# Performance work log

Measured on AMD Instinct MI355X. Metric: run time of the kernel, lower is better.

Reference implementation:

```python
import jax, jax.numpy as jnp
import numpy as np


def setup_inputs() -> dict:
    key = jax.random.key(0)
    k1, k2 = jax.random.split(key)
    B, N, C, Hq, Wq = 4, 10, 256, 32, 32
    Hs, Ws = 32, 32
    return {
        "query_features": jax.random.normal(k1, (B, C, Hq, Wq), dtype=jnp.float32),
        "support_features": jax.random.normal(k2, (N, C, Hs, Ws), dtype=jnp.float32),
        "K": 5,
    }


def reference(query_features, support_features, K):
    B, C, Hq, Wq = query_features.shape
    N, _, Hs, Ws = support_features.shape
    Lq, Ls = Hq * Wq, Hs * Ws

    # [B, Lq, C] -> repeat over N -> [B*N, Lq, C]
    q = query_features.reshape(B, C, Lq).transpose(0, 2, 1)
    q = jnp.broadcast_to(q[:, None], (B, N, Lq, C)).reshape(B * N, Lq, C)
    # [N, C, Ls] -> repeat over B -> [B*N, C, Ls]
    s = support_features.reshape(N, C, Ls)
    s = jnp.broadcast_to(s[None], (B, N, C, Ls)).reshape(B * N, C, Ls)

    # global mean-centering (scalar mean over the whole repeated tensor)
    q = q - q.mean()
    s = s - s.mean()

    # unscaled similarity attention: QK^T -> softmax -> PV
    sim = jnp.einsum("bqc,bcs->bqs", q, s)          # [B*N, Lq, Ls]
    sim = jax.nn.softmax(sim, axis=-1)
    aligned = jnp.einsum("bqs,bcs->bqc", sim, s)    # [B*N, Lq, C]

    # average over K shots per class
    aligned = aligned.reshape(B, N // K, K, Hq, Wq, C).mean(axis=2)
    aligned = aligned.transpose(1, 0, 4, 2, 3)      # [N//K, B, C, Hq, Wq]

    q_out = q.transpose(0, 2, 1).reshape(B, N // K, K, C, Hq, Wq).mean(axis=2)
    # q_out: [B, N//K, C, Hq, Wq]
    return q_out, aligned
```

## Files before the change

### kernel.cpp

```cpp
#include <hip/hip_runtime.h>

#define CQ_ELEMS (4 * 256 * 1024)
#define CS_ELEMS (10 * 256 * 1024)
#define OUT2_OFF 2097152

typedef __attribute__((ext_vector_type(8))) _Float16 f16x8;
typedef __attribute__((ext_vector_type(4))) float f32x4;

#define WS_SH 256
#define SH_ELEMS (10 * 1024 * 256)
#define SV_ELEMS (10 * 256 * 1024)

__device__ __forceinline__ void gload_lds16(const unsigned short* g, unsigned short* l) {
    __builtin_amdgcn_global_load_lds(
        (const __attribute__((address_space(1))) void*)g,
        (__attribute__((address_space(3))) void*)l, 16, 0, 0);
}

__global__ __launch_bounds__(256) void means_kernel(const float* __restrict__ q,
                                                    const float* __restrict__ s,
                                                    float* __restrict__ ws) {
    const int tid = blockIdx.x * 256 + threadIdx.x;
    const int stride = gridDim.x * 256;
    float sq = 0.f, ss = 0.f;
    const float4* q4 = (const float4*)q;
    const float4* s4 = (const float4*)s;
    for (int i = tid; i < CQ_ELEMS / 4; i += stride) {
        float4 v = q4[i];
        sq += (v.x + v.y) + (v.z + v.w);
    }
    for (int i = tid; i < CS_ELEMS / 4; i += stride) {
        float4 v = s4[i];
        ss += (v.x + v.y) + (v.z + v.w);
    }
#pragma unroll
    for (int off = 32; off > 0; off >>= 1) {
        sq += __shfl_down(sq, off, 64);
        ss += __shfl_down(ss, off, 64);
    }
    __shared__ float redq[4], reds[4];
    const int lane = threadIdx.x & 63, wid = threadIdx.x >> 6;
    if (lane == 0) { redq[wid] = sq; reds[wid] = ss; }
    __syncthreads();
    if (threadIdx.x == 0) {
        atomicAdd(&ws[0], (redq[0] + redq[1]) + (redq[2] + redq[3]));
        atomicAdd(&ws[1], (reds[0] + reds[1]) + (reds[2] + reds[3]));
    }
}

__global__ __launch_bounds__(256) void convert_kernel(const float* __restrict__ Q,
                                                      const float* __restrict__ S,
                                                      const float* __restrict__ ws,
                                                      unsigned short* __restrict__ sh,
                                                      unsigned short* __restrict__ sv,
                                                      unsigned short* __restrict__ qt,
                                                      float* __restrict__ out) {
    __shared__ unsigned short Th[32][40];
    const int t = threadIdx.x;
    const int x0 = blockIdx.x << 5;
    const int c0 = blockIdx.y << 5;
    const int z = blockIdx.z;

    const int cl = t >> 3, x4 = (t & 7) << 2;

    if (z < 10) {
        const int n = z;
        const float ms = ws[1] * (1.0f / (float)CS_ELEMS);
        float4 v = *(const float4*)(S + ((size_t)(n * 256 + c0 + cl)) * 1024 + x0 + x4);
        float x[4] = {v.x - ms, v.y - ms, v.z - ms, v.w - ms};
        unsigned short hb[4];
#pragma unroll
        for (int j = 0; j < 4; ++j) {
            _Float16 h = (_Float16)x[j];
            hb[j] = __builtin_bit_cast(unsigned short, h);
            Th[cl][x4 + j] = hb[j];
        }
        *(ushort4*)(sv + ((size_t)(n * 256 + c0 + cl)) * 1024 + x0 + x4) =
            make_ushort4(hb[0], hb[1], hb[2], hb[3]);
        {
            const int lin = (z * 8 + blockIdx.y) * 32 + blockIdx.x;
            const int gid = lin * 256 + t;
            if (gid < 524288) ((int4*)(out + OUT2_OFF))[gid] = make_int4(0, 0, 0, 0);
        }
        __syncthreads();
        const int sl = t >> 3, c4 = (t & 7) << 2;
        *(ushort4*)(sh + ((size_t)(n * 1024 + x0 + sl)) * 256 + c0 + c4) =
            make_ushort4(Th[c4 + 0][sl], Th[c4 + 1][sl], Th[c4 + 2][sl], Th[c4 + 3][sl]);
    } else {
        const int b = z - 10;
        const float mq = ws[0] * (1.0f / (float)CQ_ELEMS);
        float4 v = *(const float4*)(Q + ((size_t)(b * 256 + c0 + cl)) * 1024 + x0 + x4);
        v.x -= mq; v.y -= mq; v.z -= mq; v.w -= mq;
        float* o = out + ((size_t)(b * 2) * 256 + (c0 + cl)) * 1024 + x0 + x4;
        *(float4*)o = v;
        *(float4*)(o + 256 * 1024) = v;
        float x[4] = {v.x, v.y, v.z, v.w};
#pragma unroll
        for (int j = 0; j < 4; ++j) {
            _Float16 h = (_Float16)x[j];
            Th[cl][x4 + j] = __builtin_bit_cast(unsigned short, h);
        }
        __syncthreads();
        const int ql = t >> 3, c4 = (t & 7) << 2;
        *(ushort4*)(qt + ((size_t)(b * 1024 + x0 + ql)) * 256 + c0 + c4) =
            make_ushort4(Th[c4 + 0][ql], Th[c4 + 1][ql], Th[c4 + 2][ql], Th[c4 + 3][ql]);
    }
}

union __align__(16) SMem {
    struct {
        unsigned short s1[8192];
        unsigned short s2[8192];
        unsigned short pb[64][40];
    } st;
    float epi[2][64][68];
};

__global__ __launch_bounds__(256, 3) void attn_kernel(const unsigned short* __restrict__ qt,
                                                      const unsigned short* __restrict__ sh,
                                                      const unsigned short* __restrict__ sv,
                                                      float* __restrict__ out) {
    __shared__ SMem sm;

    const int t = threadIdx.x;
    const int w = t >> 6;
    const int lane = t & 63;
    const int quad = lane >> 4;
    const int l16 = lane & 15;

    const int q0 = blockIdx.x << 6;
    const int bn = blockIdx.y;
    const int b = bn / 10;
    const int n = bn - b * 10;
    const int g = n / 5;

    const unsigned short* __restrict__ Shn = sh + (size_t)n * (1024 * 256);
    const unsigned short* __restrict__ Svn = sv + (size_t)n * (256 * 1024);

    f16x8 qf[8];
    {
        const unsigned short* qp = qt + (size_t)(b * 1024 + q0 + 16 * w + l16) * 256 + quad * 8;
#pragma unroll
        for (int f = 0; f < 8; ++f)
            qf[f] = *(const f16x8*)(qp + f * 32);
    }

    f32x4 O[4][4];
#pragma unroll
    for (int mt = 0; mt < 4; ++mt)
#pragma unroll
        for (int nt = 0; nt < 4; ++nt) O[mt][nt] = (f32x4){0.f, 0.f, 0.f, 0.f};

    float m_run[4], l_run[4];
#pragma unroll
    for (int r = 0; r < 4; ++r) { m_run[r] = -1e30f; l_run[r] = 0.f; }

    for (int s0i = 0; s0i < 32; ++s0i) {
        const int s0 = s0i << 5;
        __syncthreads();

#pragma unroll
        for (int j = 0; j < 4; ++j) {
            const int fidx = 4 * w + j;
            const unsigned short* g1 = Shn +
                (size_t)(s0 + 2 * (lane & 15) + (fidx & 1)) * 256 + (fidx >> 1) * 32 + (lane >> 4) * 8;
            gload_lds16(g1, &sm.st.s1[fidx * 512]);
            const unsigned short* g2 = Svn +
                (size_t)(w * 64 + j * 16 + (lane >> 2)) * 1024 + s0 + ((lane & 3) ^ (lane >> 4)) * 8;
            gload_lds16(g2, &sm.st.s2[fidx * 512]);
        }
        __syncthreads();

        f32x4 sim0 = (f32x4){0.f, 0.f, 0.f, 0.f};
        f32x4 sim1 = (f32x4){0.f, 0.f, 0.f, 0.f};
#pragma unroll
        for (int f = 0; f < 8; ++f) {
            const unsigned short* base = &sm.st.s1[f * 1024 + quad * 128 + l16 * 8];
            f16x8 b0 = *(const f16x8*)base;
            f16x8 b1 = *(const f16x8*)(base + 512);
            sim0 = __builtin_amdgcn_mfma_f32_16x16x32_f16(qf[f], b0, sim0, 0, 0, 0);
            sim1 = __builtin_amdgcn_mfma_f32_16x16x32_f16(qf[f], b1, sim1, 0, 0, 0);
        }

        float rowmax[4];
#pragma unroll
        for (int r = 0; r < 4; ++r) rowmax[r] = fmaxf(sim0[r], sim1[r]);
#pragma unroll
        for (int off = 1; off <= 8; off <<= 1)
#pragma unroll
            for (int r = 0; r < 4; ++r)
                rowmax[r] = fmaxf(rowmax[r], __shfl_xor(rowmax[r], off, 64));

        float al[4], rs[4], pv0[4], pv1[4];
#pragma unroll
        for (int r = 0; r < 4; ++r) {
            const float mn = fmaxf(m_run[r], rowmax[r]);
            al[r] = __expf(m_run[r] - mn);
            m_run[r] = mn;
            pv0[r] = __expf(sim0[r] - mn);
            pv1[r] = __expf(sim1[r] - mn);
            rs[r] = pv0[r] + pv1[r];
        }
#pragma unroll
        for (int off = 1; off <= 8; off <<= 1)
#pragma unroll
            for (int r = 0; r < 4; ++r) rs[r] += __shfl_xor(rs[r], off, 64);
#pragma unroll
        for (int r = 0; r < 4; ++r) l_run[r] = l_run[r] * al[r] + rs[r];

#pragma unroll
        for (int r = 0; r < 4; ++r) {
            union { _Float16 h[2]; unsigned u; } pk;
            pk.h[0] = (_Float16)pv0[r];
            pk.h[1] = (_Float16)pv1[r];
            *(unsigned*)&sm.st.pb[16 * w + 4 * quad + r][l16 * 2] = pk.u;
        }
        if (l16 == 0) {
#pragma unroll
            for (int r = 0; r < 4; ++r)
                *(float*)&sm.st.pb[16 * w + 4 * quad + r][32] = al[r];
        }
        __syncthreads();

#pragma unroll
        for (int nt = 0; nt < 4; ++nt) {
            const float a = *(const float*)&sm.st.pb[16 * nt + l16][32];
#pragma unroll
            for (int mt = 0; mt < 4; ++mt) {
                O[mt][nt][0] *= a; O[mt][nt][1] *= a; O[mt][nt][2] *= a; O[mt][nt][3] *= a;
            }
        }
        f16x8 vf[4], pf[4];
#pragma unroll
        for (int mt = 0; mt < 4; ++mt) {
            const int c = 64 * w + 16 * mt + l16;
            const int p = c * 4 + (quad ^ ((l16 >> 2) & 3));
            vf[mt] = *(const f16x8*)&sm.st.s2[p * 8];
        }
#pragma unroll
        for (int nt = 0; nt < 4; ++nt)
            pf[nt] = *(const f16x8*)&sm.st.pb[16 * nt + l16][quad * 8];
#pragma unroll
        for (int mt = 0; mt < 4; ++mt)
#pragma unroll
            for (int nt = 0; nt < 4; ++nt)
                O[mt][nt] = __builtin_amdgcn_mfma_f32_16x16x32_f16(vf[mt], pf[nt], O[mt][nt], 0, 0, 0);
    }

    if (l16 == 0) {
#pragma unroll
        for (int r = 0; r < 4; ++r)
            *(float*)&sm.st.pb[16 * w + 4 * quad + r][34] = l_run[r];
    }
    __syncthreads();

    float linv[4];
#pragma unroll
    for (int nt = 0; nt < 4; ++nt)
        linv[nt] = 0.2f / *(const float*)&sm.st.pb[16 * nt + l16][34];
    __syncthreads();

    float* __restrict__ out2 = out + OUT2_OFF + (size_t)((g << 2) + b) * (256 * 1024);

#pragma unroll
    for (int h = 0; h < 2; ++h) {
        if ((w >> 1) == h) {
            const int we = w & 1;
#pragma unroll
            for (int mt = 0; mt < 4; ++mt)
#pragma unroll
                for (int nt = 0; nt < 4; ++nt)
#pragma unroll
                    for (int r = 0; r < 4; ++r)
                        sm.epi[we][16 * mt + 4 * quad + r][16 * nt + l16] = O[mt][nt][r] * linv[nt];
        }
        __syncthreads();
#pragma unroll 4
        for (int i = 0; i < 32; ++i) {
            const int ro = w * 32 + i;
            const float v = sm.epi[ro >> 6][ro & 63][lane];
            atomicAdd(out2 + (size_t)(h * 128 + ro) * 1024 + q0 + lane, v);
        }
        __syncthreads();
    }
}

extern "C" void kernel_launch(void* const* d_in, const int* in_sizes, int n_in,
                              void* d_out, int out_size, void* d_ws, size_t ws_size,
                              hipStream_t stream) {
    const float* q = (const float*)d_in[0];
    const float* s = (const float*)d_in[1];
    float* out = (float*)d_out;
    float* ws = (float*)d_ws;
    unsigned short* sh = (unsigned short*)((char*)d_ws + WS_SH);
    unsigned short* sv = sh + SH_ELEMS;
    unsigned short* qt = sv + SV_ELEMS;

    hipMemsetAsync(d_ws, 0, 2 * sizeof(float), stream);

    means_kernel<<<256, 256, 0, stream>>>(q, s, ws);
    convert_kernel<<<dim3(32, 8, 14), 256, 0, stream>>>(q, s, ws, sh, sv, qt, out);
    attn_kernel<<<dim3(16, 40), 256, 0, stream>>>(qt, sh, sv, out);
}
```

Measured before the change: 200.1 us.

## Double-buffer key tiles, compute softmax denominators via MFMA, and relax barriers

Key tiles (s1) are double-buffered, so the next tile's async global-to-LDS load is issued while the current tile's QK^T MFMAs run, and one barrier per iteration is dropped. The row-sum shuffle reduction is replaced by an extra MFMA with a ones matrix against the fp16 probabilities. That sum now uses fp16-rounded weights, matching what the PV product uses, and the end-of-loop LDS round trip for the denominator goes away. Manual waitcnt, s_barrier and setprio hints are added. This doubles the s1 LDS footprint, which may lower occupancy, and makes correctness depend on the hand-placed vmcnt count.

```diff
diff --git a/kernel.cpp b/kernel.cpp
--- a/kernel.cpp
+++ b/kernel.cpp
@@ -109,7 +109,7 @@
 
 union __align__(16) SMem {
     struct {
-        unsigned short s1[8192];
+        unsigned short s1[2][8192];
         unsigned short s2[8192];
         unsigned short pb[64][40];
     } st;
@@ -145,42 +145,67 @@
             qf[f] = *(const f16x8*)(qp + f * 32);
     }
 
+    f16x8 onesA;
+#pragma unroll
+    for (int j = 0; j < 8; ++j) onesA[j] = (_Float16)1.0f;
+
     f32x4 O[4][4];
 #pragma unroll
     for (int mt = 0; mt < 4; ++mt)
 #pragma unroll
         for (int nt = 0; nt < 4; ++nt) O[mt][nt] = (f32x4){0.f, 0.f, 0.f, 0.f};
 
-    float m_run[4], l_run[4];
-#pragma unroll
-    for (int r = 0; r < 4; ++r) { m_run[r] = -1e30f; l_run[r] = 0.f; }
-
+    f32x4 Lsum[4];
+#pragma unroll
+    for (int nt = 0; nt < 4; ++nt) Lsum[nt] = (f32x4){0.f, 0.f, 0.f, 0.f};
+
+    float m_run[4];
+#pragma unroll
+    for (int r = 0; r < 4; ++r) m_run[r] = -1e30f;
+
+#pragma unroll
+    for (int j = 0; j < 4; ++j) {
+        const int fidx = 4 * w + j;
+        const unsigned short* g1 = Shn +
+            (size_t)(2 * l16 + (fidx & 1)) * 256 + (fidx >> 1) * 32 + quad * 8;
+        gload_lds16(g1, &sm.st.s1[0][fidx * 512]);
+    }
+    __syncthreads();
+
+    int cur = 0;
     for (int s0i = 0; s0i < 32; ++s0i) {
         const int s0 = s0i << 5;
-        __syncthreads();
 
 #pragma unroll
         for (int j = 0; j < 4; ++j) {
             const int fidx = 4 * w + j;
-            const unsigned short* g1 = Shn +
-                (size_t)(s0 + 2 * (lane & 15) + (fidx & 1)) * 256 + (fidx >> 1) * 32 + (lane >> 4) * 8;
-            gload_lds16(g1, &sm.st.s1[fidx * 512]);
             const unsigned short* g2 = Svn +
-                (size_t)(w * 64 + j * 16 + (lane >> 2)) * 1024 + s0 + ((lane & 3) ^ (lane >> 4)) * 8;
+                (size_t)(w * 64 + j * 16 + (lane >> 2)) * 1024 + s0 + ((lane & 3) ^ quad) * 8;
             gload_lds16(g2, &sm.st.s2[fidx * 512]);
         }
-        __syncthreads();
+        {
+            const int s0n = ((s0i + 1) & 31) << 5;
+#pragma unroll
+            for (int j = 0; j < 4; ++j) {
+                const int fidx = 4 * w + j;
+                const unsigned short* g1 = Shn +
+                    (size_t)(s0n + 2 * l16 + (fidx & 1)) * 256 + (fidx >> 1) * 32 + quad * 8;
+                gload_lds16(g1, &sm.st.s1[cur ^ 1][fidx * 512]);
+            }
+        }
 
         f32x4 sim0 = (f32x4){0.f, 0.f, 0.f, 0.f};
         f32x4 sim1 = (f32x4){0.f, 0.f, 0.f, 0.f};
+        __builtin_amdgcn_s_setprio(1);
 #pragma unroll
         for (int f = 0; f < 8; ++f) {
-            const unsigned short* base = &sm.st.s1[f * 1024 + quad * 128 + l16 * 8];
+            const unsigned short* base = &sm.st.s1[cur][f * 1024 + quad * 128 + l16 * 8];
             f16x8 b0 = *(const f16x8*)base;
             f16x8 b1 = *(const f16x8*)(base + 512);
             sim0 = __builtin_amdgcn_mfma_f32_16x16x32_f16(qf[f], b0, sim0, 0, 0, 0);
             sim1 = __builtin_amdgcn_mfma_f32_16x16x32_f16(qf[f], b1, sim1, 0, 0, 0);
         }
+        __builtin_amdgcn_s_setprio(0);
 
         float rowmax[4];
 #pragma unroll
@@ -191,7 +216,7 @@
             for (int r = 0; r < 4; ++r)
                 rowmax[r] = fmaxf(rowmax[r], __shfl_xor(rowmax[r], off, 64));
 
-        float al[4], rs[4], pv0[4], pv1[4];
+        float al[4], pv0[4], pv1[4];
 #pragma unroll
         for (int r = 0; r < 4; ++r) {
             const float mn = fmaxf(m_run[r], rowmax[r]);
@@ -199,14 +224,7 @@
             m_run[r] = mn;
             pv0[r] = __expf(sim0[r] - mn);
             pv1[r] = __expf(sim1[r] - mn);
-            rs[r] = pv0[r] + pv1[r];
-        }
-#pragma unroll
-        for (int off = 1; off <= 8; off <<= 1)
-#pragma unroll
-            for (int r = 0; r < 4; ++r) rs[r] += __shfl_xor(rs[r], off, 64);
-#pragma unroll
-        for (int r = 0; r < 4; ++r) l_run[r] = l_run[r] * al[r] + rs[r];
+        }
 
 #pragma unroll
         for (int r = 0; r < 4; ++r) {
@@ -220,7 +238,9 @@
             for (int r = 0; r < 4; ++r)
                 *(float*)&sm.st.pb[16 * w + 4 * quad + r][32] = al[r];
         }
-        __syncthreads();
+        asm volatile("s_waitcnt lgkmcnt(0)" ::: "memory");
+        __builtin_amdgcn_s_barrier();
+        __builtin_amdgcn_sched_barrier(0);
 
 #pragma unroll
         for (int nt = 0; nt < 4; ++nt) {
@@ -229,7 +249,12 @@
             for (int mt = 0; mt < 4; ++mt) {
                 O[mt][nt][0] *= a; O[mt][nt][1] *= a; O[mt][nt][2] *= a; O[mt][nt][3] *= a;
             }
-        }
+            Lsum[nt][0] *= a; Lsum[nt][1] *= a; Lsum[nt][2] *= a; Lsum[nt][3] *= a;
+        }
+
+        asm volatile("s_waitcnt vmcnt(4)" ::: "memory");
+        __builtin_amdgcn_sched_barrier(0);
+
         f16x8 vf[4], pf[4];
 #pragma unroll
         for (int mt = 0; mt < 4; ++mt) {
@@ -240,25 +265,25 @@
 #pragma unroll
         for (int nt = 0; nt < 4; ++nt)
             pf[nt] = *(const f16x8*)&sm.st.pb[16 * nt + l16][quad * 8];
+        __builtin_amdgcn_s_setprio(1);
 #pragma unroll
         for (int mt = 0; mt < 4; ++mt)
 #pragma unroll
             for (int nt = 0; nt < 4; ++nt)
                 O[mt][nt] = __builtin_amdgcn_mfma_f32_16x16x32_f16(vf[mt], pf[nt], O[mt][nt], 0, 0, 0);
-    }
-
-    if (l16 == 0) {
-#pragma unroll
-        for (int r = 0; r < 4; ++r)
-            *(float*)&sm.st.pb[16 * w + 4 * quad + r][34] = l_run[r];
-    }
-    __syncthreads();
+#pragma unroll
+        for (int nt = 0; nt < 4; ++nt)
+            Lsum[nt] = __builtin_amdgcn_mfma_f32_16x16x32_f16(onesA, pf[nt], Lsum[nt], 0, 0, 0);
+        __builtin_amdgcn_s_setprio(0);
+
+        __syncthreads();
+        cur ^= 1;
+    }
 
     float linv[4];
 #pragma unroll
     for (int nt = 0; nt < 4; ++nt)
-        linv[nt] = 0.2f / *(const float*)&sm.st.pb[16 * nt + l16][34];
-    __syncthreads();
+        linv[nt] = 0.2f / Lsum[nt][0];
 
     float* __restrict__ out2 = out + OUT2_OFF + (size_t)((g << 2) + b) * (256 * 1024);
 
```

After: 271.8 us. 1.36x slower.

## Split key range across wave pairs with 32-query tiles and merged softmax

Applied to the files above, without the earlier changes.

The attention kernel now handles 32 queries per block instead of 64 and doubles the grid. The two wave pairs process alternating 32-key chunks, acting as a split-K over the key dimension. Their partial softmax states are merged at the end using the running max and sum stored in shared memory. V fragments are now read straight from global memory instead of being staged through LDS, which removes half of the LDS staging. In exchange, global traffic for V and K rises because each block covers fewer queries, and the merge adds an epilogue pass through shared memory.

```diff
diff --git a/kernel.cpp b/kernel.cpp
--- a/kernel.cpp
+++ b/kernel.cpp
@@ -109,11 +109,10 @@
 
 union __align__(16) SMem {
     struct {
-        unsigned short s1[8192];
-        unsigned short s2[8192];
-        unsigned short pb[64][40];
+        unsigned short s1g[2][8192];
+        unsigned short pbg[2][32][40];
     } st;
-    float epi[2][64][68];
+    float epi[32][265];
 };
 
 __global__ __launch_bounds__(256, 3) void attn_kernel(const unsigned short* __restrict__ qt,
@@ -121,14 +120,17 @@
                                                       const unsigned short* __restrict__ sv,
                                                       float* __restrict__ out) {
     __shared__ SMem sm;
+    __shared__ float mg[2][2][32];
 
     const int t = threadIdx.x;
     const int w = t >> 6;
+    const int h = w >> 1;
+    const int ww = w & 1;
     const int lane = t & 63;
     const int quad = lane >> 4;
     const int l16 = lane & 15;
 
-    const int q0 = blockIdx.x << 6;
+    const int q0 = blockIdx.x << 5;
     const int bn = blockIdx.y;
     const int b = bn / 10;
     const int n = bn - b * 10;
@@ -139,35 +141,32 @@
 
     f16x8 qf[8];
     {
-        const unsigned short* qp = qt + (size_t)(b * 1024 + q0 + 16 * w + l16) * 256 + quad * 8;
+        const unsigned short* qp = qt + (size_t)(b * 1024 + q0 + 16 * ww + l16) * 256 + quad * 8;
 #pragma unroll
         for (int f = 0; f < 8; ++f)
             qf[f] = *(const f16x8*)(qp + f * 32);
     }
 
-    f32x4 O[4][4];
-#pragma unroll
-    for (int mt = 0; mt < 4; ++mt)
-#pragma unroll
-        for (int nt = 0; nt < 4; ++nt) O[mt][nt] = (f32x4){0.f, 0.f, 0.f, 0.f};
+    f32x4 O[8][2];
+#pragma unroll
+    for (int mt = 0; mt < 8; ++mt)
+#pragma unroll
+        for (int nt = 0; nt < 2; ++nt) O[mt][nt] = (f32x4){0.f, 0.f, 0.f, 0.f};
 
     float m_run[4], l_run[4];
 #pragma unroll
     for (int r = 0; r < 4; ++r) { m_run[r] = -1e30f; l_run[r] = 0.f; }
 
-    for (int s0i = 0; s0i < 32; ++s0i) {
-        const int s0 = s0i << 5;
-        __syncthreads();
-
-#pragma unroll
-        for (int j = 0; j < 4; ++j) {
-            const int fidx = 4 * w + j;
+    for (int s0i = 0; s0i < 16; ++s0i) {
+        const int s0 = (2 * s0i + h) << 5;
+        __syncthreads();
+
+#pragma unroll
+        for (int j = 0; j < 8; ++j) {
+            const int fidx = 8 * ww + j;
             const unsigned short* g1 = Shn +
-                (size_t)(s0 + 2 * (lane & 15) + (fidx & 1)) * 256 + (fidx >> 1) * 32 + (lane >> 4) * 8;
-            gload_lds16(g1, &sm.st.s1[fidx * 512]);
-            const unsigned short* g2 = Svn +
-                (size_t)(w * 64 + j * 16 + (lane >> 2)) * 1024 + s0 + ((lane & 3) ^ (lane >> 4)) * 8;
-            gload_lds16(g2, &sm.st.s2[fidx * 512]);
+                (size_t)(s0 + 2 * l16 + (fidx & 1)) * 256 + (fidx >> 1) * 32 + quad * 8;
+            gload_lds16(g1, &sm.st.s1g[h][fidx * 512]);
         }
         __syncthreads();
 
@@ -175,7 +174,7 @@
         f32x4 sim1 = (f32x4){0.f, 0.f, 0.f, 0.f};
 #pragma unroll
         for (int f = 0; f < 8; ++f) {
-            const unsigned short* base = &sm.st.s1[f * 1024 + quad * 128 + l16 * 8];
+            const unsigned short* base = &sm.st.s1g[h][f * 1024 + quad * 128 + l16 * 8];
             f16x8 b0 = *(const f16x8*)base;
             f16x8 b1 = *(const f16x8*)(base + 512);
             sim0 = __builtin_amdgcn_mfma_f32_16x16x32_f16(qf[f], b0, sim0, 0, 0, 0);
@@ -210,78 +209,93 @@
 
 #pragma unroll
         for (int r = 0; r < 4; ++r) {
-            union { _Float16 h[2]; unsigned u; } pk;
-            pk.h[0] = (_Float16)pv0[r];
-            pk.h[1] = (_Float16)pv1[r];
-            *(unsigned*)&sm.st.pb[16 * w + 4 * quad + r][l16 * 2] = pk.u;
+            union { _Float16 hh[2]; unsigned u; } pk;
+            pk.hh[0] = (_Float16)pv0[r];
+            pk.hh[1] = (_Float16)pv1[r];
+            *(unsigned*)&sm.st.pbg[h][16 * ww + 4 * quad + r][l16 * 2] = pk.u;
         }
         if (l16 == 0) {
 #pragma unroll
             for (int r = 0; r < 4; ++r)
-                *(float*)&sm.st.pb[16 * w + 4 * quad + r][32] = al[r];
-        }
-        __syncthreads();
-
-#pragma unroll
-        for (int nt = 0; nt < 4; ++nt) {
-            const float a = *(const float*)&sm.st.pb[16 * nt + l16][32];
-#pragma unroll
-            for (int mt = 0; mt < 4; ++mt) {
+                *(float*)&sm.st.pbg[h][16 * ww + 4 * quad + r][32] = al[r];
+        }
+        __syncthreads();
+
+#pragma unroll
+        for (int nt = 0; nt < 2; ++nt) {
+            const float a = *(const float*)&sm.st.pbg[h][16 * nt + l16][32];
+#pragma unroll
+            for (int mt = 0; mt < 8; ++mt) {
                 O[mt][nt][0] *= a; O[mt][nt][1] *= a; O[mt][nt][2] *= a; O[mt][nt][3] *= a;
             }
         }
-        f16x8 vf[4], pf[4];
-#pragma unroll
-        for (int mt = 0; mt < 4; ++mt) {
-            const int c = 64 * w + 16 * mt + l16;
-            const int p = c * 4 + (quad ^ ((l16 >> 2) & 3));
-            vf[mt] = *(const f16x8*)&sm.st.s2[p * 8];
-        }
-#pragma unroll
-        for (int nt = 0; nt < 4; ++nt)
-            pf[nt] = *(const f16x8*)&sm.st.pb[16 * nt + l16][quad * 8];
-#pragma unroll
-        for (int mt = 0; mt < 4; ++mt)
-#pragma unroll
-            for (int nt = 0; nt < 4; ++nt)
+
+        f16x8 vf[8], pf[2];
+#pragma unroll
+        for (int mt = 0; mt < 8; ++mt)
+            vf[mt] = *(const f16x8*)(Svn + (size_t)(128 * ww + 16 * mt + l16) * 1024 + s0 + quad * 8);
+#pragma unroll
+        for (int nt = 0; nt < 2; ++nt)
+            pf[nt] = *(const f16x8*)&sm.st.pbg[h][16 * nt + l16][quad * 8];
+#pragma unroll
+        for (int mt = 0; mt < 8; ++mt)
+#pragma unroll
+            for (int nt = 0; nt < 2; ++nt)
                 O[mt][nt] = __builtin_amdgcn_mfma_f32_16x16x32_f16(vf[mt], pf[nt], O[mt][nt], 0, 0, 0);
     }
 
+    __syncthreads();
     if (l16 == 0) {
 #pragma unroll
-        for (int r = 0; r < 4; ++r)
-            *(float*)&sm.st.pb[16 * w + 4 * quad + r][34] = l_run[r];
-    }
-    __syncthreads();
-
-    float linv[4];
-#pragma unroll
-    for (int nt = 0; nt < 4; ++nt)
-        linv[nt] = 0.2f / *(const float*)&sm.st.pb[16 * nt + l16][34];
+        for (int r = 0; r < 4; ++r) {
+            mg[0][h][16 * ww + 4 * quad + r] = m_run[r];
+            mg[1][h][16 * ww + 4 * quad + r] = l_run[r];
+        }
+    }
+    __syncthreads();
+
+    float fsc[2];
+#pragma unroll
+    for (int nt = 0; nt < 2; ++nt) {
+        const int qrow = 16 * nt + l16;
+        const float m0 = mg[0][0][qrow], m1 = mg[0][1][qrow];
+        const float l0 = mg[1][0][qrow], l1 = mg[1][1][qrow];
+        const float ms = fmaxf(m0, m1);
+        const float e0 = __expf(m0 - ms), e1 = __expf(m1 - ms);
+        const float lT = l0 * e0 + l1 * e1;
+        fsc[nt] = (h ? e1 : e0) * 0.2f / lT;
+    }
+
+    if (h == 1) {
+#pragma unroll
+        for (int mt = 0; mt < 8; ++mt)
+#pragma unroll
+            for (int nt = 0; nt < 2; ++nt)
+#pragma unroll
+                for (int r = 0; r < 4; ++r)
+                    sm.epi[16 * nt + l16][128 * ww + 16 * mt + 4 * quad + r] = O[mt][nt][r] * fsc[nt];
+    }
+    __syncthreads();
+    if (h == 0) {
+#pragma unroll
+        for (int mt = 0; mt < 8; ++mt)
+#pragma unroll
+            for (int nt = 0; nt < 2; ++nt)
+#pragma unroll
+                for (int r = 0; r < 4; ++r)
+                    sm.epi[16 * nt + l16][128 * ww + 16 * mt + 4 * quad + r] += O[mt][nt][r] * fsc[nt];
+    }
     __syncthreads();
 
     float* __restrict__ out2 = out + OUT2_OFF + (size_t)((g << 2) + b) * (256 * 1024);
-
-#pragma unroll
-    for (int h = 0; h < 2; ++h) {
-        if ((w >> 1) == h) {
-            const int we = w & 1;
-#pragma unroll
-            for (int mt = 0; mt < 4; ++mt)
-#pragma unroll
-                for (int nt = 0; nt < 4; ++nt)
-#pragma unroll
-                    for (int r = 0; r < 4; ++r)
-                        sm.epi[we][16 * mt + 4 * quad + r][16 * nt + l16] = O[mt][nt][r] * linv[nt];
-        }
-        __syncthreads();
+    {
+        const int q = lane & 31;
+        const int codd = lane >> 5;
 #pragma unroll 4
         for (int i = 0; i < 32; ++i) {
-            const int ro = w * 32 + i;
-            const float v = sm.epi[ro >> 6][ro & 63][lane];
-            atomicAdd(out2 + (size_t)(h * 128 + ro) * 1024 + q0 + lane, v);
-        }
-        __syncthreads();
+            const int c = 64 * w + 2 * i + codd;
+            atomicAdd(out2 + (size_t)c * 1024 + q0 + q, sm.epi[q][c]);
+        }
     }
 }
 
@@ -300,5 +314,5 @@
 
     means_kernel<<<256, 256, 0, stream>>>(q, s, ws);
     convert_kernel<<<dim3(32, 8, 14), 256, 0, stream>>>(q, s, ws, sh, sv, qt, out);
-    attn_kernel<<<dim3(16, 40), 256, 0, stream>>>(qt, sh, sv, out);
-}
+    attn_kernel<<<dim3(32, 40), 256, 0, stream>>>(qt, sh, sv, out);
+}
```

Result: slower. 285.3 us (+42.6%).

## Compute softmax row sums via MFMA with ones and remap block order for locality

Applied to the files above, without the earlier changes.

Drops the per-tile shuffle reduction of softmax row sums. The sums now come from an extra MFMA that multiplies an all-ones operand by the fp16 probability tile, rescaled together with the output accumulator, which also removes the LDS round trip for l_run and a barrier. The grid is flattened to 1D and remapped so that consecutive blocks share the same support index n, aiming for better L2 reuse of support tiles. The row sum now uses the fp16-rounded probabilities, which matches what the PV product uses, and adds 4 MFMAs plus extra accumulator registers per iteration.

```diff
diff --git a/kernel.cpp b/kernel.cpp
--- a/kernel.cpp
+++ b/kernel.cpp
@@ -128,10 +128,24 @@
     const int quad = lane >> 4;
     const int l16 = lane & 15;
 
-    const int q0 = blockIdx.x << 6;
-    const int bn = blockIdx.y;
-    const int b = bn / 10;
-    const int n = bn - b * 10;
+    int qx, b, n;
+    {
+        const int L = blockIdx.x;
+        if (L < 512) {
+            n = L & 7;
+            const int inner = L >> 3;
+            b = inner & 3;
+            qx = inner >> 2;
+        } else {
+            const int r = L - 512;
+            const int x = r & 7;
+            n = 8 + (x >> 2);
+            const int combo = (x & 3) * 16 + (r >> 3);
+            b = combo & 3;
+            qx = combo >> 2;
+        }
+    }
+    const int q0 = qx << 6;
     const int g = n / 5;
 
     const unsigned short* __restrict__ Shn = sh + (size_t)n * (1024 * 256);
@@ -145,15 +159,23 @@
             qf[f] = *(const f16x8*)(qp + f * 32);
     }
 
+    f16x8 onesA;
+#pragma unroll
+    for (int j = 0; j < 8; ++j) onesA[j] = (_Float16)1.0f;
+
     f32x4 O[4][4];
 #pragma unroll
     for (int mt = 0; mt < 4; ++mt)
 #pragma unroll
         for (int nt = 0; nt < 4; ++nt) O[mt][nt] = (f32x4){0.f, 0.f, 0.f, 0.f};
 
-    float m_run[4], l_run[4];
-#pragma unroll
-    for (int r = 0; r < 4; ++r) { m_run[r] = -1e30f; l_run[r] = 0.f; }
+    f32x4 Lsum[4];
+#pragma unroll
+    for (int nt = 0; nt < 4; ++nt) Lsum[nt] = (f32x4){0.f, 0.f, 0.f, 0.f};
+
+    float m_run[4];
+#pragma unroll
+    for (int r = 0; r < 4; ++r) m_run[r] = -1e30f;
 
     for (int s0i = 0; s0i < 32; ++s0i) {
         const int s0 = s0i << 5;
@@ -191,7 +213,7 @@
             for (int r = 0; r < 4; ++r)
                 rowmax[r] = fmaxf(rowmax[r], __shfl_xor(rowmax[r], off, 64));
 
-        float al[4], rs[4], pv0[4], pv1[4];
+        float al[4], pv0[4], pv1[4];
 #pragma unroll
         for (int r = 0; r < 4; ++r) {
             const float mn = fmaxf(m_run[r], rowmax[r]);
@@ -199,14 +221,7 @@
             m_run[r] = mn;
             pv0[r] = __expf(sim0[r] - mn);
             pv1[r] = __expf(sim1[r] - mn);
-            rs[r] = pv0[r] + pv1[r];
-        }
-#pragma unroll
-        for (int off = 1; off <= 8; off <<= 1)
-#pragma unroll
-            for (int r = 0; r < 4; ++r) rs[r] += __shfl_xor(rs[r], off, 64);
-#pragma unroll
-        for (int r = 0; r < 4; ++r) l_run[r] = l_run[r] * al[r] + rs[r];
+        }
 
 #pragma unroll
         for (int r = 0; r < 4; ++r) {
@@ -229,6 +244,7 @@
             for (int mt = 0; mt < 4; ++mt) {
                 O[mt][nt][0] *= a; O[mt][nt][1] *= a; O[mt][nt][2] *= a; O[mt][nt][3] *= a;
             }
+            Lsum[nt][0] *= a; Lsum[nt][1] *= a; Lsum[nt][2] *= a; Lsum[nt][3] *= a;
         }
         f16x8 vf[4], pf[4];
 #pragma unroll
@@ -245,20 +261,17 @@
 #pragma unroll
             for (int nt = 0; nt < 4; ++nt)
                 O[mt][nt] = __builtin_amdgcn_mfma_f32_16x16x32_f16(vf[mt], pf[nt], O[mt][nt], 0, 0, 0);
-    }
-
-    if (l16 == 0) {
-#pragma unroll
-        for (int r = 0; r < 4; ++r)
-            *(float*)&sm.st.pb[16 * w + 4 * quad + r][34] = l_run[r];
-    }
+#pragma unroll
+        for (int nt = 0; nt < 4; ++nt)
+            Lsum[nt] = __builtin_amdgcn_mfma_f32_16x16x32_f16(onesA, pf[nt], Lsum[nt], 0, 0, 0);
+    }
+
     __syncthreads();
 
     float linv[4];
 #pragma unroll
     for (int nt = 0; nt < 4; ++nt)
-        linv[nt] = 0.2f / *(const float*)&sm.st.pb[16 * nt + l16][34];
-    __syncthreads();
+        linv[nt] = 0.2f / Lsum[nt][0];
 
     float* __restrict__ out2 = out + OUT2_OFF + (size_t)((g << 2) + b) * (256 * 1024);
 
@@ -300,5 +313,5 @@
 
     means_kernel<<<256, 256, 0, stream>>>(q, s, ws);
     convert_kernel<<<dim3(32, 8, 14), 256, 0, stream>>>(q, s, ws, sh, sv, qt, out);
-    attn_kernel<<<dim3(16, 40), 256, 0, stream>>>(qt, sh, sv, out);
-}
+    attn_kernel<<<640, 256, 0, stream>>>(qt, sh, sv, out);
+}
```

Measured after the change: 190.8 us. 1.05x faster.
